# Kernel optimization log

Hardware: AMD Instinct MI355X
Metric: run time of the kernel (lower is better)

The kernel has to match this reference:

```python
import jax, jax.numpy as jnp
import numpy as np

NUM_PAGES = 1048576
TOKENS_PER_PAGE = 32
SLOTS = 256
MAX_PAGES_PER_SLOT = 4096
MAX_SEQ = 65536  # <= max_pages_per_slot*tokens_per_page/2, leaves room to grow


def setup_inputs() -> dict:
    key = jax.random.key(0)
    k1, = jax.random.split(key, 1)
    # random current sequence lengths per slot (some may be 0 / inactive)
    seq = jax.random.randint(k1, (SLOTS,), 0, MAX_SEQ).astype(jnp.int32)
    npu = (seq + TOKENS_PER_PAGE - 1) // TOKENS_PER_PAGE  # ceil-div pages used
    cols = jnp.arange(MAX_PAGES_PER_SLOT, dtype=jnp.int32)
    # give slot i the disjoint page-id range [1 + i*2048, ...); valid since
    # max pages/slot here = ceil(65535/32) = 2048 and 1+255*2048+2047 < NUM_PAGES
    pm = jnp.where(
        cols[None, :] < npu[:, None],
        1 + jnp.arange(SLOTS, dtype=jnp.int32)[:, None] * 2048 + cols[None, :],
        -1,
    ).astype(jnp.int32)
    # mark exactly the mapped pages as in-use (index 0 used as a safe dump slot)
    safe_idx = jnp.where(pm > -1, pm, 0)
    vals = (pm > -1).astype(jnp.int32)
    page_status = jnp.zeros((NUM_PAGES,), jnp.int32).at[safe_idx].max(vals)
    page_status = page_status.at[0].set(0)
    current_page = jnp.where(
        npu > 0,
        jnp.take_along_axis(pm, jnp.maximum(npu - 1, 0)[:, None], axis=1)[:, 0],
        -1,
    ).astype(jnp.int32)
    cpp = jnp.where(seq == 0, 0, (seq - 1) % TOKENS_PER_PAGE).astype(jnp.int32)
    return {
        "page_status": page_status,
        "page_map": pm,
        "sequence_lengths": seq,
        "num_pages_used": npu.astype(jnp.int32),
        "current_page": current_page,
        "current_page_position": cpp,
    }


def _find_next_free_page(page_status):
    # matches PageManager.find_next_free_page: first free index in [1, N), else 0
    free = jnp.where(page_status[1:] == 0, size=1, fill_value=-1)[0] + 1
    return free[0].astype(jnp.int32)


def reference(page_status, page_map, sequence_lengths, num_pages_used,
              current_page, current_page_position):
    """Faithful port of PageManager.reserve_decode_step_pages (autoregressive step)."""
    tpp = TOKENS_PER_PAGE
    new_seq = sequence_lengths + jnp.where(current_page == -1, 0, 1).astype(jnp.int32)
    new_npu = (new_seq + tpp - 1) // tpp
    new_cpp = jnp.where(new_seq == 0, 0, (new_seq - 1) % tpp).astype(jnp.int32)

    def step(carry, i):
        ps, pm, cp = carry
        needs_new_page = new_npu[i] > num_pages_used[i]
        nfp = jax.lax.cond(
            needs_new_page,
            lambda: _find_next_free_page(ps),
            lambda: jnp.int32(-1),
        )
        ps = jax.lax.cond(needs_new_page, lambda x: x.at[nfp].set(1), lambda x: x, ps)
        pm = jax.lax.cond(
            needs_new_page,
            lambda x: x.at[i, num_pages_used[i]].set(nfp),
            lambda x: x,
            pm,
        )
        cp = jax.lax.cond(needs_new_page, lambda x: x.at[i].set(nfp), lambda x: x, cp)
        return (ps, pm, cp), None

    (ps, pm, cp), _ = jax.lax.scan(
        step, (page_status, page_map, current_page), jnp.arange(SLOTS, dtype=jnp.int32)
    )
    # PageState fields in declaration order
    return (ps, pm, new_seq, new_npu.astype(jnp.int32), cp, new_cpp)
```

## Files before the change

### kernel.cpp

```cpp
#include <hip/hip_runtime.h>

#define NUM_PAGES 1048576
#define TPP 32
#define SLOTS 256
#define MPPS 4096
#define NBLK 1024
#define NTHR 256

__global__ __launch_bounds__(NTHR) void fused(
    const int* __restrict__ ps, const int* __restrict__ pm,
    const int* __restrict__ seq, const int* __restrict__ npu,
    const int* __restrict__ cp, int* __restrict__ out)
{
    const int t = threadIdx.x, b = blockIdx.x;
    const int lane = t & 63, wave = t >> 6;
    const unsigned long long mlt = (1ULL << lane) - 1ULL;

    int* out_ps  = out;
    int* out_pm  = out + NUM_PAGES;
    int* out_seq = out + 2 * NUM_PAGES;
    int* out_npu = out_seq + SLOTS;
    int* out_cp  = out_npu + SLOTS;
    int* out_cpp = out_cp + SLOTS;

    __shared__ int s_w[4];
    __shared__ int s_free[SLOTS];
    __shared__ int s_found;

    const int gi = b * NTHR + t;
    const int4 pv = reinterpret_cast<const int4*>(ps)[gi];
    const int4 mv = reinterpret_cast<const int4*>(pm)[gi];

    int sq = seq[t], c = cp[t], u = npu[t];
    int ns = sq + (c != -1);
    int nn = (ns + TPP - 1) / TPP;
    int ncpp = (ns == 0) ? 0 : ((ns - 1) & (TPP - 1));
    int needs = (nn > u) ? 1 : 0;
    unsigned long long bal = __ballot(needs);
    if (lane == 0) s_w[wave] = __popcll(bal);
    if (t == 0) s_found = 0;
    __syncthreads();
    int woff = 0;
    for (int w = 0; w < wave; ++w) woff += s_w[w];
    const int r = woff + __popcll(bal & mlt);
    const int K = s_w[0] + s_w[1] + s_w[2] + s_w[3];
    __syncthreads();

    for (int base = 0; base < NUM_PAGES && s_found < K; base += 4 * NTHR) {
        int4 v = reinterpret_cast<const int4*>(ps)[(base >> 2) + t];
        int m = ((v.x == 0) ? 1 : 0) | ((v.y == 0) ? 2 : 0) |
                ((v.z == 0) ? 4 : 0) | ((v.w == 0) ? 8 : 0);
        if (base == 0 && t == 0) m &= ~1;
        int q = __popc(m);
        int x = q;
        for (int o = 1; o < 64; o <<= 1) { int y = __shfl_up(x, o); if (lane >= o) x += y; }
        if (lane == 63) s_w[wave] = x;
        __syncthreads();
        int wo = 0;
        for (int w = 0; w < wave; ++w) wo += s_w[w];
        int pos = s_found + wo + x - q;
        #pragma unroll
        for (int j = 0; j < 4; ++j) if (m & (1 << j)) {
            int p = pos + __popc(m & ((1 << j) - 1));
            if (p < K) s_free[p] = base + t * 4 + j;
        }
        __syncthreads();
        if (t == 0) s_found += s_w[0] + s_w[1] + s_w[2] + s_w[3];
        __syncthreads();
    }
    const int fe = (s_found < K) ? s_found : K;

    reinterpret_cast<int4*>(out_ps)[gi] = pv;
    reinterpret_cast<int4*>(out_pm)[gi] = mv;
    __syncthreads();

    const int nfp = (needs && r < fe) ? s_free[r] : 0;
    if (b == 0) {
        out_seq[t] = ns;
        out_npu[t] = nn;
        out_cpp[t] = ncpp;
        out_cp[t]  = needs ? nfp : c;
    }
    if (needs && t == (b >> 2) && (u >> 10) == (b & 3))
        out_pm[t * MPPS + u] = nfp;
    if (t < K) {
        int f = (t < fe) ? s_free[t] : 0;
        if ((f >> 10) == b) out_ps[f] = 1;
    }
}

extern "C" void kernel_launch(void* const* d_in, const int* in_sizes, int n_in,
                              void* d_out, int out_size, void* d_ws, size_t ws_size,
                              hipStream_t stream)
{
    const int* page_status = (const int*)d_in[0];
    const int* page_map    = (const int*)d_in[1];
    const int* seq         = (const int*)d_in[2];
    const int* npu         = (const int*)d_in[3];
    const int* cp          = (const int*)d_in[4];

    fused<<<NBLK, NTHR, 0, stream>>>(
        page_status, page_map, seq, npu, cp, (int*)d_out);
}
```

Baseline: 10.56 us.

## Run free-page scan in a single wave with prefetched status and no block barriers

The free-page search moves from a block-wide loop, which took three __syncthreads per round, into wave 0 alone. Wave 0 uses warp shuffles for its prefix sums and prefetches the first 2048 page_status entries into registers before scanning. Per-slot metadata is loaded as int4 by one wave and passed to the other threads through shared memory, and the other waves just copy their slice of page_status and page_map. This removes barrier overhead on the serial scan, at the cost of scanning 256 pages per round instead of 1024 and leaving the other waves idle.

New measurement: 11.08 us. 4.9% more time.

```diff
diff --git a/kernel.cpp b/kernel.cpp
--- a/kernel.cpp
+++ b/kernel.cpp
@@ -7,6 +7,8 @@
 #define NBLK 1024
 #define NTHR 256
 
+#define ELEM(v, j) ((j) == 0 ? (v).x : (j) == 1 ? (v).y : (j) == 2 ? (v).z : (v).w)
+
 __global__ __launch_bounds__(NTHR) void fused(
     const int* __restrict__ ps, const int* __restrict__ pm,
     const int* __restrict__ seq, const int* __restrict__ npu,
@@ -14,7 +16,6 @@
 {
     const int t = threadIdx.x, b = blockIdx.x;
     const int lane = t & 63, wave = t >> 6;
-    const unsigned long long mlt = (1ULL << lane) - 1ULL;
 
     int* out_ps  = out;
     int* out_pm  = out + NUM_PAGES;
@@ -23,69 +24,111 @@
     int* out_cp  = out_npu + SLOTS;
     int* out_cpp = out_cp + SLOTS;
 
-    __shared__ int s_w[4];
     __shared__ int s_free[SLOTS];
-    __shared__ int s_found;
+    __shared__ int s_info[SLOTS];
+    __shared__ int s_col[SLOTS];
+    __shared__ int s_cpo[SLOTS];
+    __shared__ int s_K, s_fe;
 
+    const int4* ps4 = reinterpret_cast<const int4*>(ps);
     const int gi = b * NTHR + t;
-    const int4 pv = reinterpret_cast<const int4*>(ps)[gi];
-    const int4 mv = reinterpret_cast<const int4*>(pm)[gi];
 
-    int sq = seq[t], c = cp[t], u = npu[t];
-    int ns = sq + (c != -1);
-    int nn = (ns + TPP - 1) / TPP;
-    int ncpp = (ns == 0) ? 0 : ((ns - 1) & (TPP - 1));
-    int needs = (nn > u) ? 1 : 0;
-    unsigned long long bal = __ballot(needs);
-    if (lane == 0) s_w[wave] = __popcll(bal);
-    if (t == 0) s_found = 0;
-    __syncthreads();
-    int woff = 0;
-    for (int w = 0; w < wave; ++w) woff += s_w[w];
-    const int r = woff + __popcll(bal & mlt);
-    const int K = s_w[0] + s_w[1] + s_w[2] + s_w[3];
+    if (wave == 0) {
+        const int4 sq4 = reinterpret_cast<const int4*>(seq)[lane];
+        const int4 cq4 = reinterpret_cast<const int4*>(cp)[lane];
+        const int4 nu4 = reinterpret_cast<const int4*>(npu)[lane];
+        int4 pc[8];
+        #pragma unroll
+        for (int r = 0; r < 8; ++r) pc[r] = ps4[r * 64 + lane];
+        const int4 pv = ps4[gi];
+        const int4 mv = reinterpret_cast<const int4*>(pm)[gi];
+
+        int ns0, ns1, ns2, ns3, nn0, nn1, nn2, nn3, nb = 0;
+        ns0 = sq4.x + (cq4.x != -1); nn0 = (ns0 + TPP - 1) / TPP; if (nn0 > nu4.x) nb |= 1;
+        ns1 = sq4.y + (cq4.y != -1); nn1 = (ns1 + TPP - 1) / TPP; if (nn1 > nu4.y) nb |= 2;
+        ns2 = sq4.z + (cq4.z != -1); nn2 = (ns2 + TPP - 1) / TPP; if (nn2 > nu4.z) nb |= 4;
+        ns3 = sq4.w + (cq4.w != -1); nn3 = (ns3 + TPP - 1) / TPP; if (nn3 > nu4.w) nb |= 8;
+
+        if (b == 0) {
+            int4 o;
+            o.x = ns0; o.y = ns1; o.z = ns2; o.w = ns3;
+            reinterpret_cast<int4*>(out_seq)[lane] = o;
+            o.x = nn0; o.y = nn1; o.z = nn2; o.w = nn3;
+            reinterpret_cast<int4*>(out_npu)[lane] = o;
+            o.x = (ns0 == 0) ? 0 : ((ns0 - 1) & (TPP - 1));
+            o.y = (ns1 == 0) ? 0 : ((ns1 - 1) & (TPP - 1));
+            o.z = (ns2 == 0) ? 0 : ((ns2 - 1) & (TPP - 1));
+            o.w = (ns3 == 0) ? 0 : ((ns3 - 1) & (TPP - 1));
+            reinterpret_cast<int4*>(out_cpp)[lane] = o;
+        }
+
+        int cnt = __popc(nb), x = cnt;
+        #pragma unroll
+        for (int o = 1; o < 64; o <<= 1) { int y = __shfl_up(x, o); if (lane >= o) x += y; }
+        const int K = __shfl(x, 63);
+        const int base_r = x - cnt;
+        int4 iv;
+        iv.x = (nb & 1) ? base_r : -1;
+        iv.y = (nb & 2) ? base_r + __popc(nb & 1) : -1;
+        iv.z = (nb & 4) ? base_r + __popc(nb & 3) : -1;
+        iv.w = (nb & 8) ? base_r + __popc(nb & 7) : -1;
+        reinterpret_cast<int4*>(s_info)[lane] = iv;
+        reinterpret_cast<int4*>(s_col)[lane]  = nu4;
+        reinterpret_cast<int4*>(s_cpo)[lane]  = cq4;
+
+        auto doRound = [&](int4 v, int pagebase, int sf) -> int {
+            int m = ((v.x == 0) ? 1 : 0) | ((v.y == 0) ? 2 : 0) |
+                    ((v.z == 0) ? 4 : 0) | ((v.w == 0) ? 8 : 0);
+            if (pagebase == 0 && lane == 0) m &= ~1;
+            int q = __popc(m), xx = q;
+            #pragma unroll
+            for (int o = 1; o < 64; o <<= 1) { int y = __shfl_up(xx, o); if (lane >= o) xx += y; }
+            int pos = sf + xx - q;
+            #pragma unroll
+            for (int j = 0; j < 4; ++j) if (m & (1 << j)) {
+                int p = pos + __popc(m & ((1 << j) - 1));
+                if (p < K) s_free[p] = pagebase + lane * 4 + j;
+            }
+            return sf + __shfl(xx, 63);
+        };
+
+        int sf = 0;
+        #pragma unroll
+        for (int r = 0; r < 8; ++r)
+            if (sf < K) sf = doRound(pc[r], r * 256, sf);
+        for (int pb = 2048; pb < NUM_PAGES && sf < K; pb += 256)
+            sf = doRound(ps4[(pb >> 2) + lane], pb, sf);
+
+        if (lane == 0) { s_K = K; s_fe = (sf < K) ? sf : K; }
+
+        reinterpret_cast<int4*>(out_ps)[gi] = pv;
+        reinterpret_cast<int4*>(out_pm)[gi] = mv;
+    } else {
+        const int4 pv = ps4[gi];
+        const int4 mv = reinterpret_cast<const int4*>(pm)[gi];
+        reinterpret_cast<int4*>(out_ps)[gi] = pv;
+        reinterpret_cast<int4*>(out_pm)[gi] = mv;
+    }
+
     __syncthreads();
 
-    for (int base = 0; base < NUM_PAGES && s_found < K; base += 4 * NTHR) {
-        int4 v = reinterpret_cast<const int4*>(ps)[(base >> 2) + t];
-        int m = ((v.x == 0) ? 1 : 0) | ((v.y == 0) ? 2 : 0) |
-                ((v.z == 0) ? 4 : 0) | ((v.w == 0) ? 8 : 0);
-        if (base == 0 && t == 0) m &= ~1;
-        int q = __popc(m);
-        int x = q;
-        for (int o = 1; o < 64; o <<= 1) { int y = __shfl_up(x, o); if (lane >= o) x += y; }
-        if (lane == 63) s_w[wave] = x;
-        __syncthreads();
-        int wo = 0;
-        for (int w = 0; w < wave; ++w) wo += s_w[w];
-        int pos = s_found + wo + x - q;
-        #pragma unroll
-        for (int j = 0; j < 4; ++j) if (m & (1 << j)) {
-            int p = pos + __popc(m & ((1 << j) - 1));
-            if (p < K) s_free[p] = base + t * 4 + j;
-        }
-        __syncthreads();
-        if (t == 0) s_found += s_w[0] + s_w[1] + s_w[2] + s_w[3];
-        __syncthreads();
-    }
-    const int fe = (s_found < K) ? s_found : K;
+    const int K = s_K, fe = s_fe;
 
-    reinterpret_cast<int4*>(out_ps)[gi] = pv;
-    reinterpret_cast<int4*>(out_pm)[gi] = mv;
-    __syncthreads();
-
-    const int nfp = (needs && r < fe) ? s_free[r] : 0;
-    if (b == 0) {
-        out_seq[t] = ns;
-        out_npu[t] = nn;
-        out_cpp[t] = ncpp;
-        out_cp[t]  = needs ? nfp : c;
-    }
-    if (needs && t == (b >> 2) && (u >> 10) == (b & 3))
-        out_pm[t * MPPS + u] = nfp;
     if (t < K) {
         int f = (t < fe) ? s_free[t] : 0;
         if ((f >> 10) == b) out_ps[f] = 1;
+    }
+    if (t == 64) {
+        int slot = b >> 2, info = s_info[slot];
+        if (info >= 0) {
+            int col = s_col[slot];
+            if ((col >> 10) == (b & 3))
+                out_pm[slot * MPPS + col] = (info < fe) ? s_free[info] : 0;
+        }
+    }
+    if (b == 0) {
+        int info = s_info[t];
+        out_cp[t] = (info >= 0) ? ((info < fe) ? s_free[info] : 0) : s_cpo[t];
     }
 }
 
```
